# Performance work log

Measured on AMD Instinct MI355X. Metric: run time of the kernel, lower is better.

Reference implementation:

```python
import jax, jax.numpy as jnp
import numpy as np

B, S, D, H, HD = 2, 2048, 2048, 16, 128
MAX_TIMESCALE = 10000.0


def _fixed_pos_embedding(features, length, max_timescale):
    # flaxformer embedding.generate_fixed_pos_embedding
    fraction = jnp.arange(0, features, 2, dtype=jnp.float32) / features
    timescale = max_timescale ** fraction  # min_timescale = 1.0
    sinusoid = jnp.einsum('i,j->ij', jnp.arange(length, dtype=jnp.float32), 1.0 / timescale)
    sinusoid = jnp.concatenate([sinusoid, sinusoid], axis=-1)  # [length, features]
    return jnp.sin(sinusoid), jnp.cos(sinusoid)


def _rotate_half(x):
    x1, x2 = jnp.split(x, 2, axis=-1)
    return jnp.concatenate([-x2, x1], axis=-1)


def _apply_rope(x, sin, cos):
    # x: [B, S, H, HD]; sin/cos: [S, HD]
    sin = sin[None, :, None, :].astype(x.dtype)
    cos = cos[None, :, None, :].astype(x.dtype)
    return x * cos + _rotate_half(x) * sin


def setup_inputs() -> dict:
    key = jax.random.key(0)
    ks = jax.random.split(key, 6)
    inputs_q = jax.random.normal(ks[0], (B, S, D), dtype=jnp.float32)
    inputs_kv = jax.random.normal(ks[1], (B, S, D), dtype=jnp.float32)
    scale = D ** -0.5
    wq = jax.random.normal(ks[2], (D, H, HD), dtype=jnp.float32) * scale
    wk = jax.random.normal(ks[3], (D, H, HD), dtype=jnp.float32) * scale
    wv = jax.random.normal(ks[4], (D, H, HD), dtype=jnp.float32) * scale
    wo = jax.random.normal(ks[5], (H, HD, D), dtype=jnp.float32) * ((H * HD) ** -0.5)
    mask = jnp.tril(jnp.ones((S, S), dtype=bool))[None, None]  # causal [1,1,S,S]
    return {"inputs_q": inputs_q, "inputs_kv": inputs_kv, "wq": wq, "wk": wk,
            "wv": wv, "wo": wo, "mask": mask}


def reference(inputs_q, inputs_kv, wq, wk, wv, wo, mask):
    # QKV projections (split-head kernels) -> [B, S, H, HD]
    q = jnp.einsum('bqd,dhf->bqhf', inputs_q, wq)
    k = jnp.einsum('bkd,dhf->bkhf', inputs_kv, wk)
    v = jnp.einsum('bkd,dhf->bkhf', inputs_kv, wv)

    # Rotary embeddings applied to full head dim (fraction_to_rotate = 1.0)
    sin, cos = _fixed_pos_embedding(HD, S, MAX_TIMESCALE)
    q = _apply_rope(q, sin, cos)
    k = _apply_rope(k, sin, cos)

    # Logit rescaling by 1/sqrt(head_dim) (rescale_logits=False default path)
    q = q * (HD ** -0.5)

    logits = jnp.einsum('bqhf,bkhf->bhqk', q, k)  # [B, H, S, S]
    logits = jnp.where(mask, logits, jnp.asarray(-1e10, logits.dtype))
    probs = jax.nn.softmax(logits, axis=-1)

    ctx = jnp.einsum('bhqk,bkhf->bqhf', probs, v)
    out = jnp.einsum('bqhf,hfd->bqd', ctx, wo)  # output projection
    return out
```

## Files before the change

### kernel.cpp

```cpp
#include <hip/hip_runtime.h>

#define S_LEN 2048
#define NH 16
#define HDIM 128
#define DMODEL 2048

typedef __attribute__((ext_vector_type(8))) short bf16x8;
typedef __attribute__((ext_vector_type(4))) float f32x4;

using gas_cvp = const __attribute__((address_space(1))) void*;
using las_vp  = __attribute__((address_space(3))) void*;

__device__ __forceinline__ unsigned short f2bf(float x) {
  unsigned int u = __builtin_bit_cast(unsigned int, x);
  u += 0x7FFFu + ((u >> 16) & 1u);
  return (unsigned short)(u >> 16);
}
__device__ __forceinline__ float bf2f(unsigned short u) {
  unsigned int x = ((unsigned int)u) << 16;
  return __builtin_bit_cast(float, x);
}
__device__ __forceinline__ unsigned int cvt_pk_bf16(float lo, float hi) {
  unsigned int r;
  asm("v_cvt_pk_bf16_f32 %0, %1, %2" : "=v"(r) : "v"(lo), "v"(hi));
  return r;
}

__global__ __launch_bounds__(256) void cvt2_kernel(const float4* __restrict__ inq,
                                                   const float4* __restrict__ inkv,
                                                   ushort4* __restrict__ outq,
                                                   ushort4* __restrict__ outkv, int n4) {
  const float4* in = blockIdx.z ? inkv : inq;
  ushort4* out = blockIdx.z ? outkv : outq;
  int i = blockIdx.x * 256 + threadIdx.x;
  if (i < n4) {
    float4 v = in[i];
    ushort4 r;
    r.x = f2bf(v.x); r.y = f2bf(v.y); r.z = f2bf(v.z); r.w = f2bf(v.w);
    out[i] = r;
  }
}

__global__ __launch_bounds__(256) void sincos_kernel(float2* __restrict__ sc) {
  int i = blockIdx.x * 256 + threadIdx.x;
  int s = i >> 6, j = i & 63;
  float inv_ts = 1.0f / powf(10000.0f, (float)j * (1.0f / 64.0f));
  float ang = (float)s * inv_ts;
  sc[i] = make_float2(sinf(ang), cosf(ang));
}

__global__ __launch_bounds__(256) void rope8_kernel(const unsigned short* __restrict__ XQ,
                                                    const unsigned short* __restrict__ XK,
                                                    const float2* __restrict__ sc,
                                                    unsigned short* __restrict__ outQ,
                                                    unsigned short* __restrict__ outK,
                                                    float qscale) {
  const unsigned short* X = blockIdx.z ? XK : XQ;
  unsigned short* out = blockIdx.z ? outK : outQ;
  float scale = blockIdx.z ? 1.0f : qscale;
  int i = blockIdx.x * 256 + threadIdx.x;
  int m = i >> 7;
  int r = i & 127;
  int h = r >> 3, jb = (r & 7) * 8;
  int s = m & (S_LEN - 1);
  size_t base = (size_t)m * DMODEL + h * HDIM + jb;
  int4 x1 = *(const int4*)(X + base);
  int4 x2 = *(const int4*)(X + base + 64);
  const float2* pp = sc + s * 64 + jb;
  int4 o1, o2;
  int* x1w = (int*)&x1; int* x2w = (int*)&x2;
  int* o1w = (int*)&o1; int* o2w = (int*)&o2;
#pragma unroll
  for (int w = 0; w < 4; w++) {
    float a_lo = bf2f((unsigned short)(x1w[w] & 0xffff));
    float a_hi = bf2f((unsigned short)((unsigned int)x1w[w] >> 16));
    float b_lo = bf2f((unsigned short)(x2w[w] & 0xffff));
    float b_hi = bf2f((unsigned short)((unsigned int)x2w[w] >> 16));
    float2 c0 = pp[w * 2], c1 = pp[w * 2 + 1];
    float r1l = (a_lo * c0.y - b_lo * c0.x) * scale;
    float r1h = (a_hi * c1.y - b_hi * c1.x) * scale;
    float r2l = (b_lo * c0.y + a_lo * c0.x) * scale;
    float r2h = (b_hi * c1.y + a_hi * c1.x) * scale;
    o1w[w] = (int)(cvt_pk_bf16(r1l, r1h));
    o2w[w] = (int)(cvt_pk_bf16(r2l, r2h));
  }
  *(int4*)(out + base) = o1;
  *(int4*)(out + base + 64) = o2;
}

__global__ __launch_bounds__(256) void wtrans4_kernel(const float* __restrict__ w0,
                                                      const float* __restrict__ w1,
                                                      const float* __restrict__ w2,
                                                      const float* __restrict__ w3,
                                                      unsigned short* __restrict__ outb) {
  __shared__ float tile[64][65];
  int z = blockIdx.z;
  const float* in = (z == 0) ? w0 : (z == 1) ? w1 : (z == 2) ? w2 : w3;
  unsigned short* out = outb + (size_t)z * DMODEL * DMODEL;
  int c0 = blockIdx.x * 64, r0 = blockIdx.y * 64;
  int tx = threadIdx.x & 63, ty = threadIdx.x >> 6;
#pragma unroll
  for (int i = 0; i < 16; i++) {
    int r = ty + i * 4;
    tile[r][tx] = in[(size_t)(r0 + r) * DMODEL + c0 + tx];
  }
  __syncthreads();
#pragma unroll
  for (int i = 0; i < 16; i++) {
    int c = ty + i * 4;
    out[(size_t)(c0 + c) * DMODEL + r0 + tx] = f2bf(tile[tx][c]);
  }
}

__global__ __launch_bounds__(256) void vtrans_kernel(const unsigned short* __restrict__ vf,
                                                     unsigned short* __restrict__ Vt) {
  __shared__ unsigned short tile[64][65];
  int z = blockIdx.z; int b = z >> 4, h = z & 15;
  const unsigned short* I = vf + (size_t)b * S_LEN * DMODEL + h * HDIM;
  unsigned short* O = Vt + (size_t)z * HDIM * S_LEN;
  int s0 = blockIdx.y * 64, f0 = blockIdx.x * 64;
  int tx = threadIdx.x & 63, ty = threadIdx.x >> 6;
#pragma unroll
  for (int i = 0; i < 16; i++) {
    int r = ty + i * 4;
    tile[r][tx] = I[(size_t)(s0 + r) * DMODEL + f0 + tx];
  }
  __syncthreads();
#pragma unroll
  for (int i = 0; i < 16; i++) {
    int c = ty + i * 4;
    O[(size_t)(f0 + c) * S_LEN + s0 + tx] = tile[tx][c];
  }
}

__global__ __launch_bounds__(512, 1) void gemm256o_kernel(
    const unsigned short* __restrict__ Aq,
    const unsigned short* __restrict__ Akv,
    const unsigned short* __restrict__ W,
    unsigned short* __restrict__ Cb) {
  constexpr int M = 4096, N = 2048, K = 2048, NT = K / 64;
  __shared__ char lds[131072];
  int wid = blockIdx.z * 128 + blockIdx.y * 8 + blockIdx.x;
  int nid = (wid & 7) * 32 + (wid >> 3);
  int z = nid >> 7;
  int rem = nid & 127;
  int bm = (rem >> 3) * 256, bn = (rem & 7) * 256;
  const unsigned short* A = (z == 0) ? Aq : Akv;
  const unsigned short* Bt = W + (size_t)z * N * K;

  int tid = threadIdx.x, wave = tid >> 6, lane = tid & 63;
  int lr = lane & 15, lq = lane >> 4;
  int wr = wave >> 2, wc = wave & 3;

  auto STAGE_P = [&](int t, int buf, int isB) {
    int k0 = t * 64;
    const unsigned short* src = isB ? Bt : A;
    int rbase = isB ? bn : bm;
    char* dst0 = lds + buf * 65536 + isB * 32768;
#pragma unroll
    for (int i = 0; i < 4; i++) {
      int o = i * 8192 + tid * 16;
      int row = o >> 7, colb = o & 127;
      int sc = colb ^ ((row & 7) << 4);
      __builtin_amdgcn_global_load_lds(
          (gas_cvp)(src + (size_t)(rbase + row) * K + k0 + (sc >> 1)),
          (las_vp)(dst0 + i * 8192 + wave * 1024), 16, 0, 0);
    }
  };
  auto LDA1 = [&](int buf, int m, int kk) -> bf16x8 {
    int row = wr * 128 + m * 16 + lr;
    return *(const bf16x8*)(lds + buf * 65536 + row * 128 +
                            (((kk * 4 + lq) ^ (row & 7)) << 4));
  };
  auto LDB1 = [&](int buf, int n, int kk) -> bf16x8 {
    int row = wc * 64 + n * 16 + lr;
    return *(const bf16x8*)(lds + buf * 65536 + 32768 + row * 128 +
                            (((kk * 4 + lq) ^ (row & 7)) << 4));
  };

  f32x4 acc[8][4] = {};
  bf16x8 aA[4][2], bB[4][2];

  auto OCT = [&](int P, int Q, int sb) {
#pragma unroll
    for (int kk = 0; kk < 2; kk++)
#pragma unroll
      for (int s = 0; s < 2; s++)
#pragma unroll
        for (int nn = 0; nn < 2; nn++)
          acc[2 * P + s][2 * Q + nn] = __builtin_amdgcn_mfma_f32_16x16x32_bf16(
              aA[sb + s][kk], bB[2 * Q + nn][kk], acc[2 * P + s][2 * Q + nn], 0, 0, 0);
  };
  auto RD_A2 = [&](int buf, int m0, int sb) {
#pragma unroll
    for (int kk = 0; kk < 2; kk++)
#pragma unroll
      for (int s = 0; s < 2; s++) aA[sb + s][kk] = LDA1(buf, m0 + s, kk);
  };
  auto RD_B2 = [&](int buf, int n0) {
#pragma unroll
    for (int kk = 0; kk < 2; kk++)
#pragma unroll
      for (int s = 0; s < 2; s++) bB[n0 + s][kk] = LDB1(buf, n0 + s, kk);
  };

  STAGE_P(0, 0, 0); STAGE_P(0, 0, 1);
  asm volatile("s_waitcnt vmcnt(0)" ::: "memory");
  __builtin_amdgcn_sched_barrier(0);

  for (int T = 0; T < NT; T++) {
    int c = T & 1, nc = c ^ 1;
    __builtin_amdgcn_s_barrier();
    if (T + 1 < NT) { STAGE_P(T + 1, nc, 0); STAGE_P(T + 1, nc, 1); }
    __builtin_amdgcn_sched_barrier(0);
    RD_A2(c, 0, 0);
    __builtin_amdgcn_sched_barrier(0);
    RD_B2(c, 0);
    __builtin_amdgcn_sched_barrier(0);
    RD_B2(c, 2);
    __builtin_amdgcn_sched_barrier(0);
    RD_A2(c, 2, 2);
    __builtin_amdgcn_sched_barrier(0);

    asm volatile("s_waitcnt lgkmcnt(8)" ::: "memory");
    __builtin_amdgcn_sched_barrier(0);
    __builtin_amdgcn_s_setprio(1);
    OCT(0, 0, 0);
    __builtin_amdgcn_s_setprio(0);
    asm volatile("s_waitcnt lgkmcnt(4)" ::: "memory");
    __builtin_amdgcn_sched_barrier(0);
    __builtin_amdgcn_s_setprio(1);
    OCT(0, 1, 0);
    __builtin_amdgcn_s_setprio(0);
    RD_A2(c, 4, 0);
    __builtin_amdgcn_sched_barrier(0);
    asm volatile("s_waitcnt lgkmcnt(4)" ::: "memory");
    __builtin_amdgcn_sched_barrier(0);
    __builtin_amdgcn_s_setprio(1);
    OCT(1, 0, 2); OCT(1, 1, 2);
    __builtin_amdgcn_s_setprio(0);
    RD_A2(c, 6, 2);
    __builtin_amdgcn_sched_barrier(0);
    asm volatile("s_waitcnt lgkmcnt(4)" ::: "memory");
    __builtin_amdgcn_sched_barrier(0);
    __builtin_amdgcn_s_setprio(1);
    OCT(2, 0, 0); OCT(2, 1, 0);
    __builtin_amdgcn_s_setprio(0);
    asm volatile("s_waitcnt lgkmcnt(0)" ::: "memory");
    __builtin_amdgcn_sched_barrier(0);
    __builtin_amdgcn_s_setprio(1);
    OCT(3, 0, 2); OCT(3, 1, 2);
    __builtin_amdgcn_s_setprio(0);
    if (T + 1 < NT) {
      asm volatile("s_waitcnt vmcnt(0)" ::: "memory");
      __builtin_amdgcn_sched_barrier(0);
    }
  }
  asm volatile("s_waitcnt vmcnt(0) lgkmcnt(0)" ::: "memory");

  unsigned short* C = Cb + (size_t)z * M * N;
#pragma unroll
  for (int m = 0; m < 8; m++)
#pragma unroll
    for (int n = 0; n < 4; n++) {
      int row0 = bm + wr * 128 + m * 16 + lq * 4;
      int col = bn + wc * 64 + n * 16 + lr;
#pragma unroll
      for (int r = 0; r < 4; r++)
        C[(size_t)(row0 + r) * N + col] = f2bf(acc[m][n][r]);
    }
}

template <bool BF16OUT>
__global__ __launch_bounds__(512, 1) void gemmk_kernel(
    const unsigned short* __restrict__ Aq,
    const unsigned short* __restrict__ Akv,
    const unsigned short* __restrict__ W,
    void* __restrict__ Cb) {
  constexpr int M = 4096, N = 2048, K = 2048, NT = K / 64;
  __shared__ char lds[147456];
  int z = blockIdx.z;
  const unsigned short* A = (z == 0) ? Aq : Akv;
  const unsigned short* Bt = W + (size_t)z * N * K;

  int wid = blockIdx.y * 16 + blockIdx.x;
  int nid = (wid & 7) * 32 + (wid >> 3);
  int bn = (nid & 15) * 128, bm = (nid >> 4) * 256;

  int tid = threadIdx.x, wave = tid >> 6, lane = tid & 63;
  int lr = lane & 15, lq = lane >> 4;
  int wr = wave >> 1, wc = wave & 1;

  auto STAGE_U = [&](int t, int buf, int which) {
    int k0 = t * 64;
    const unsigned short* src = (which < 2) ? A : Bt;
    int rbase = (which < 2) ? (bm + which * 128) : bn;
    char* dst0 = lds + buf * 49152 + which * 16384;
#pragma unroll
    for (int i = 0; i < 2; i++) {
      int o = i * 8192 + wave * 1024 + lane * 16;
      int row = o >> 7, colb = o & 127;
      int sc = colb ^ ((row & 7) << 4);
      __builtin_amdgcn_global_load_lds(
          (gas_cvp)(src + (size_t)(rbase + row) * K + k0 + (sc >> 1)),
          (las_vp)(dst0 + i * 8192 + wave * 1024), 16, 0, 0);
    }
  };
  auto LDA = [&](int buf, int m, int kk) -> bf16x8 {
    int row = wr * 64 + m * 16 + lr;
    int half = row >> 7, r = row & 127;
    int byt = r * 128 + (((kk * 4 + lq) ^ (r & 7)) << 4);
    return *(const bf16x8*)(lds + buf * 49152 + half * 16384 + byt);
  };
  auto LDB = [&](int buf, int n, int kk) -> bf16x8 {
    int row = wc * 64 + n * 16 + lr;
    int byt = row * 128 + (((kk * 4 + lq) ^ (row & 7)) << 4);
    return *(const bf16x8*)(lds + buf * 49152 + 32768 + byt);
  };

  f32x4 acc[4][4] = {};
  bf16x8 aA[4][2], bB[4][2];

  auto QUAD = [&](int mg, int ng) {
#pragma unroll
    for (int kk = 0; kk < 2; kk++)
#pragma unroll
      for (int mm = 0; mm < 2; mm++)
#pragma unroll
        for (int nn = 0; nn < 2; nn++)
          acc[mg * 2 + mm][ng * 2 + nn] = __builtin_amdgcn_mfma_f32_16x16x32_bf16(
              aA[mg * 2 + mm][kk], bB[ng * 2 + nn][kk], acc[mg * 2 + mm][ng * 2 + nn], 0, 0, 0);
  };

  auto BODY = [&](int T, int cur, int dst, int mode) {
    __builtin_amdgcn_s_barrier();
    if (mode == 0) {
      STAGE_U(T + 2, dst, 0); STAGE_U(T + 2, dst, 1); STAGE_U(T + 2, dst, 2);
    }
    __builtin_amdgcn_sched_barrier(0);
#pragma unroll
    for (int kk = 0; kk < 2; kk++)
#pragma unroll
      for (int mm = 0; mm < 2; mm++) aA[mm][kk] = LDA(cur, mm, kk);
#pragma unroll
    for (int kk = 0; kk < 2; kk++)
#pragma unroll
      for (int nn = 0; nn < 2; nn++) bB[nn][kk] = LDB(cur, nn, kk);
    __builtin_amdgcn_sched_barrier(0);
#pragma unroll
    for (int kk = 0; kk < 2; kk++)
#pragma unroll
      for (int nn = 0; nn < 2; nn++) bB[2 + nn][kk] = LDB(cur, 2 + nn, kk);
    __builtin_amdgcn_sched_barrier(0);
#pragma unroll
    for (int kk = 0; kk < 2; kk++)
#pragma unroll
      for (int mm = 0; mm < 2; mm++) aA[2 + mm][kk] = LDA(cur, 2 + mm, kk);
    __builtin_amdgcn_sched_barrier(0);

    asm volatile("s_waitcnt lgkmcnt(8)" ::: "memory");
    __builtin_amdgcn_sched_barrier(0);
    __builtin_amdgcn_s_setprio(1);
    QUAD(0, 0);
    __builtin_amdgcn_s_setprio(0);
    asm volatile("s_waitcnt lgkmcnt(4)" ::: "memory");
    __builtin_amdgcn_sched_barrier(0);
    __builtin_amdgcn_s_setprio(1);
    QUAD(0, 1);
    __builtin_amdgcn_s_setprio(0);
    asm volatile("s_waitcnt lgkmcnt(0)" ::: "memory");
    __builtin_amdgcn_sched_barrier(0);
    __builtin_amdgcn_s_setprio(1);
    QUAD(1, 0); QUAD(1, 1);
    __builtin_amdgcn_s_setprio(0);
    if (mode == 0)      asm volatile("s_waitcnt vmcnt(6)" ::: "memory");
    else if (mode == 1) asm volatile("s_waitcnt vmcnt(0)" ::: "memory");
    __builtin_amdgcn_sched_barrier(0);
  };

  STAGE_U(0, 0, 0); STAGE_U(0, 0, 1); STAGE_U(0, 0, 2);
  STAGE_U(1, 1, 0); STAGE_U(1, 1, 1); STAGE_U(1, 1, 2);
  asm volatile("s_waitcnt vmcnt(6)" ::: "memory");
  __builtin_amdgcn_sched_barrier(0);

  int cur = 0;
  for (int T = 0; T < NT - 2; T++) {
    int dst = (cur == 0) ? 2 : cur - 1;
    BODY(T, cur, dst, 0);
    cur = (cur == 2) ? 0 : cur + 1;
  }
  BODY(NT - 2, cur, 0, 1);
  cur = (cur == 2) ? 0 : cur + 1;
  BODY(NT - 1, cur, 0, 2);
  asm volatile("s_waitcnt vmcnt(0) lgkmcnt(0)" ::: "memory");

#pragma unroll
  for (int m = 0; m < 4; m++)
#pragma unroll
    for (int n = 0; n < 4; n++) {
      int row0 = bm + wr * 64 + m * 16 + lq * 4;
      int col = bn + wc * 64 + n * 16 + lr;
      if (BF16OUT) {
        unsigned short* C = (unsigned short*)Cb;
#pragma unroll
        for (int r = 0; r < 4; r++)
          C[(size_t)(row0 + r) * N + col] = f2bf(acc[m][n][r]);
      } else {
        float* C = (float*)Cb;
#pragma unroll
        for (int r = 0; r < 4; r++)
          C[(size_t)(row0 + r) * N + col] = acc[m][n][r];
      }
    }
}

__global__ __launch_bounds__(512, 4) void attn_kernel(const unsigned short* __restrict__ Qb,
                                                      const unsigned short* __restrict__ Kb,
                                                      const unsigned short* __restrict__ Vt,
                                                      unsigned short* __restrict__ ctx) {
  __shared__ char lds[65536];
  int d = blockIdx.x;
  int hb = d & 31;
  int rank = d >> 5;
  int qtile = (rank < 8) ? (15 - rank) : (rank - 8);
  int h = hb & 15, b = hb >> 4;

  int tid = threadIdx.x, wave = tid >> 6, lane = tid & 63;
  int lr = lane & 15, lq = lane >> 4;
  int qw = qtile * 128 + wave * 16;
  int nt = 2 * qtile + 2;

  const unsigned short* Qp = Qb + (size_t)b * S_LEN * DMODEL + (size_t)h * HDIM;
  const unsigned short* Kp = Kb + (size_t)b * S_LEN * DMODEL + (size_t)h * HDIM;
  const unsigned short* Vp = Vt + (size_t)(b * NH + h) * HDIM * S_LEN;

  bf16x8 qa[4];
#pragma unroll
  for (int kf = 0; kf < 4; kf++)
    qa[kf] = *(const bf16x8*)(Qp + (size_t)(qw + lr) * DMODEL + kf * 32 + lq * 8);

  f32x4 o[8] = {};
  float mrow = -1e30f;
  float lsum = 0.f;
  bool hi = (lane >= 32);
  bool odd = (lq & 1);

  auto STAGE = [&](int tt, int bsel) {
    int kk0 = tt * 64;
#pragma unroll
    for (int i = 0; i < 2; i++) {
      int o_ = wave * 2048 + i * 1024 + lane * 16;
      int row = o_ >> 8, colb = o_ & 255;
      int sc_ = colb ^ ((row & 7) << 4);
      __builtin_amdgcn_global_load_lds(
          (gas_cvp)(Kp + (size_t)(kk0 + row) * DMODEL + (sc_ >> 1)),
          (las_vp)(lds + bsel * 32768 + wave * 2048 + i * 1024), 16, 0, 0);
    }
#pragma unroll
    for (int i = 0; i < 2; i++) {
      int o_ = wave * 2048 + i * 1024 + lane * 16;
      int row = o_ >> 7, colb = o_ & 127;
      int sc_ = colb ^ ((row & 7) << 4);
      __builtin_amdgcn_global_load_lds(
          (gas_cvp)(Vp + (size_t)row * S_LEN + kk0 + (sc_ >> 1)),
          (las_vp)(lds + bsel * 32768 + 16384 + wave * 2048 + i * 1024), 16, 0, 0);
    }
  };

  STAGE(0, 0);
  __syncthreads();

  for (int t = 0; t < nt; t++) {
    int cur = t & 1;
    int k0 = t * 64;
    if (t + 1 < nt) STAGE(t + 1, cur ^ 1);

    bool active = (k0 <= qw + 15);
    if (active) {
      const char* kbb = lds + cur * 32768;
      f32x4 sf[4] = {};
#pragma unroll
      for (int kf = 0; kf < 4; kf++) {
        bf16x8 kbf[4];
#pragma unroll
        for (int nf = 0; nf < 4; nf++) {
          int row = nf * 16 + lr;
          int colb = kf * 64 + lq * 16;
          kbf[nf] = *(const bf16x8*)(kbb + row * 256 + (colb ^ ((row & 7) << 4)));
        }
#pragma unroll
        for (int nf = 0; nf < 4; nf++)
          sf[nf] = __builtin_amdgcn_mfma_f32_16x16x32_bf16(kbf[nf], qa[kf], sf[nf], 0, 0, 0);
      }

      if (k0 + 63 > qw) {
        int q = qw + lr;
#pragma unroll
        for (int nf = 0; nf < 4; nf++)
#pragma unroll
          for (int r = 0; r < 4; r++)
            if (k0 + nf * 16 + lq * 4 + r > q) sf[nf][r] = -1e30f;
      }

      float v = sf[0][0];
#pragma unroll
      for (int nf = 0; nf < 4; nf++)
#pragma unroll
        for (int r = 0; r < 4; r++) v = fmaxf(v, sf[nf][r]);
      v = fmaxf(v, __shfl_xor(v, 16));
      v = fmaxf(v, __shfl_xor(v, 32));
      bool need = (v > mrow + 8.f);
      if (__any(need)) {
        float mn = fmaxf(mrow, v);
        float al = exp2f(mrow - mn);
        mrow = mn;
        lsum *= al;
#pragma unroll
        for (int ff = 0; ff < 8; ff++) o[ff] *= al;
      }
      float rs = 0.f;
#pragma unroll
      for (int nf = 0; nf < 4; nf++)
#pragma unroll
        for (int r = 0; r < 4; r++) {
          float p = exp2f(sf[nf][r] - mrow);
          sf[nf][r] = p;
          rs += p;
        }
      rs += __shfl_xor(rs, 16);
      rs += __shfl_xor(rs, 32);
      lsum += rs;

      const char* vbb = lds + cur * 32768 + 16384;
#pragma unroll
      for (int c = 0; c < 2; c++) {
        unsigned int A0 = cvt_pk_bf16(sf[2 * c][0], sf[2 * c][1]);
        unsigned int A1 = cvt_pk_bf16(sf[2 * c][2], sf[2 * c][3]);
        unsigned int B0 = cvt_pk_bf16(sf[2 * c + 1][0], sf[2 * c + 1][1]);
        unsigned int B1 = cvt_pk_bf16(sf[2 * c + 1][2], sf[2 * c + 1][3]);
        unsigned int sA0 = (unsigned int)__shfl_xor((int)A0, 32);
        unsigned int sA1 = (unsigned int)__shfl_xor((int)A1, 32);
        unsigned int sB0 = (unsigned int)__shfl_xor((int)B0, 32);
        unsigned int sB1 = (unsigned int)__shfl_xor((int)B1, 32);
        unsigned int Y0f = hi ? sB0 : A0, Y0s = hi ? B0 : sA0;
        unsigned int Y1f = hi ? sB1 : A1, Y1s = hi ? B1 : sA1;
        unsigned int z0 = odd ? Y0f : Y0s, z1 = odd ? Y1f : Y1s;
        unsigned int w0 = (unsigned int)__shfl_xor((int)z0, 16);
        unsigned int w1 = (unsigned int)__shfl_xor((int)z1, 16);
        int4 fr;
        fr.x = (int)(odd ? w0 : Y0f);
        fr.y = (int)(odd ? w1 : Y1f);
        fr.z = (int)(odd ? Y0s : w0);
        fr.w = (int)(odd ? Y1s : w1);
        bf16x8 pfrag = __builtin_bit_cast(bf16x8, fr);
#pragma unroll
        for (int ff = 0; ff < 8; ff++) {
          int row = ff * 16 + lr;
          int colb = c * 64 + lq * 16;
          bf16x8 vb = *(const bf16x8*)(vbb + row * 128 + (colb ^ ((row & 7) << 4)));
          o[ff] = __builtin_amdgcn_mfma_f32_16x16x32_bf16(vb, pfrag, o[ff], 0, 0, 0);
        }
      }
    }

    __syncthreads();
  }

  float inv = 1.0f / lsum;
  size_t rb = ((size_t)b * S_LEN + qw + lr) * DMODEL + h * HDIM;
#pragma unroll
  for (int ff = 0; ff < 8; ff++) {
    unsigned int u0 = cvt_pk_bf16(o[ff][0] * inv, o[ff][1] * inv);
    unsigned int u1 = cvt_pk_bf16(o[ff][2] * inv, o[ff][3] * inv);
    *(uint2*)(ctx + rb + ff * 16 + lq * 4) = make_uint2(u0, u1);
  }
}

extern "C" void kernel_launch(void* const* d_in, const int* in_sizes, int n_in,
                              void* d_out, int out_size, void* d_ws, size_t ws_size,
                              hipStream_t stream) {
  const float* inq  = (const float*)d_in[0];
  const float* inkv = (const float*)d_in[1];
  const float* wq   = (const float*)d_in[2];
  const float* wk   = (const float*)d_in[3];
  const float* wv   = (const float*)d_in[4];
  const float* wo   = (const float*)d_in[5];
  float* out = (float*)d_out;

  char* ws = (char*)d_ws;
  const size_t MB = 1ull << 20;
  unsigned short* xq  = (unsigned short*)(ws);
  unsigned short* xkv = (unsigned short*)(ws + 16 * MB);
  unsigned short* wqt = (unsigned short*)(ws + 32 * MB);
  unsigned short* wvt = (unsigned short*)(ws + 48 * MB);
  unsigned short* wot = (unsigned short*)(ws + 56 * MB);
  float2* sc          = (float2*)(ws + 64 * MB);
  unsigned short* projb = (unsigned short*)(ws + 66 * MB);
  unsigned short* Vt   = (unsigned short*)(ws + 114 * MB);
  unsigned short* ctxb = (unsigned short*)(ws + 130 * MB);
  unsigned short* Qb = xq;
  unsigned short* Kb = xkv;

  const int n4 = (2 * S_LEN * DMODEL) / 4;
  cvt2_kernel<<<dim3(n4 / 256, 1, 2), 256, 0, stream>>>(
      (const float4*)inq, (const float4*)inkv, (ushort4*)xq, (ushort4*)xkv, n4);

  wtrans4_kernel<<<dim3(32, 32, 4), 256, 0, stream>>>(wq, wk, wv, wo, wqt);

  sincos_kernel<<<(S_LEN * 64) / 256, 256, 0, stream>>>(sc);

  const float qscale = 0.12751743249052045f;
  unsigned short* projQ = projb;
  unsigned short* projK = projb + (size_t)4096 * 2048;
  unsigned short* projV = projb + (size_t)2 * 4096 * 2048;

  gemm256o_kernel<<<dim3(8, 16, 2), 512, 0, stream>>>(xq, xkv, wqt, projb);
  gemmk_kernel<true><<<dim3(16, 16, 1), 512, 0, stream>>>(xkv, xkv, wvt, (void*)projV);

  rope8_kernel<<<dim3(2048, 1, 2), 256, 0, stream>>>(projQ, projK, sc, Qb, Kb, qscale);
  vtrans_kernel<<<dim3(2, 32, 32), 256, 0, stream>>>(projV, Vt);

  attn_kernel<<<512, 512, 0, stream>>>(Qb, Kb, Vt, ctxb);

  gemmk_kernel<false><<<dim3(16, 16, 1), 512, 0, stream>>>(ctxb, ctxb, wot, (void*)out);
}
```

Measured before the change: 259.5 us.

## Switch GEMMs to 32x32x16 MFMA tiles and compute softmax row sums via MFMA

Both projection GEMM kernels move from 16x16x32 to 32x32x16 bf16 MFMA fragments. Each K-step is restructured into alternating X/Y register fragment sets, and the LDS swizzle now also XORs in row bits 3-4, so the wider fragment reads do not hit bank conflicts. Larger MFMA tiles cut the number of LDS fragment loads per FLOP. In attention, the per-row softmax sum is computed with an extra MFMA against a ones vector instead of scalar adds and cross-lane shuffles. The epilogue store layouts change to the 32x32 accumulator layout, and the wider accumulators raise register pressure.

```diff
diff --git a/kernel.cpp b/kernel.cpp
--- a/kernel.cpp
+++ b/kernel.cpp
@@ -7,6 +7,7 @@
 
 typedef __attribute__((ext_vector_type(8))) short bf16x8;
 typedef __attribute__((ext_vector_type(4))) float f32x4;
+typedef __attribute__((ext_vector_type(16))) float f32x16;
 
 using gas_cvp = const __attribute__((address_space(1))) void*;
 using las_vp  = __attribute__((address_space(3))) void*;
@@ -24,6 +25,9 @@
   unsigned int r;
   asm("v_cvt_pk_bf16_f32 %0, %1, %2" : "=v"(r) : "v"(lo), "v"(hi));
   return r;
+}
+__device__ __forceinline__ int gswz(int row) {
+  return (((row & 7) ^ ((row >> 3) & 3)) << 4);
 }
 
 __global__ __launch_bounds__(256) void cvt2_kernel(const float4* __restrict__ inq,
@@ -149,7 +153,7 @@
   const unsigned short* Bt = W + (size_t)z * N * K;
 
   int tid = threadIdx.x, wave = tid >> 6, lane = tid & 63;
-  int lr = lane & 15, lq = lane >> 4;
+  int l31 = lane & 31, l5 = lane >> 5;
   int wr = wave >> 2, wc = wave & 3;
 
   auto STAGE_P = [&](int t, int buf, int isB) {
@@ -161,47 +165,51 @@
     for (int i = 0; i < 4; i++) {
       int o = i * 8192 + tid * 16;
       int row = o >> 7, colb = o & 127;
-      int sc = colb ^ ((row & 7) << 4);
+      int sc = colb ^ gswz(row);
       __builtin_amdgcn_global_load_lds(
           (gas_cvp)(src + (size_t)(rbase + row) * K + k0 + (sc >> 1)),
           (las_vp)(dst0 + i * 8192 + wave * 1024), 16, 0, 0);
     }
   };
-  auto LDA1 = [&](int buf, int m, int kk) -> bf16x8 {
-    int row = wr * 128 + m * 16 + lr;
-    return *(const bf16x8*)(lds + buf * 65536 + row * 128 +
-                            (((kk * 4 + lq) ^ (row & 7)) << 4));
-  };
-  auto LDB1 = [&](int buf, int n, int kk) -> bf16x8 {
-    int row = wc * 64 + n * 16 + lr;
-    return *(const bf16x8*)(lds + buf * 65536 + 32768 + row * 128 +
-                            (((kk * 4 + lq) ^ (row & 7)) << 4));
-  };
-
-  f32x4 acc[8][4] = {};
-  bf16x8 aA[4][2], bB[4][2];
-
-  auto OCT = [&](int P, int Q, int sb) {
-#pragma unroll
-    for (int kk = 0; kk < 2; kk++)
-#pragma unroll
-      for (int s = 0; s < 2; s++)
-#pragma unroll
-        for (int nn = 0; nn < 2; nn++)
-          acc[2 * P + s][2 * Q + nn] = __builtin_amdgcn_mfma_f32_16x16x32_bf16(
-              aA[sb + s][kk], bB[2 * Q + nn][kk], acc[2 * P + s][2 * Q + nn], 0, 0, 0);
-  };
-  auto RD_A2 = [&](int buf, int m0, int sb) {
-#pragma unroll
-    for (int kk = 0; kk < 2; kk++)
-#pragma unroll
-      for (int s = 0; s < 2; s++) aA[sb + s][kk] = LDA1(buf, m0 + s, kk);
-  };
-  auto RD_B2 = [&](int buf, int n0) {
-#pragma unroll
-    for (int kk = 0; kk < 2; kk++)
-#pragma unroll
-      for (int s = 0; s < 2; s++) bB[n0 + s][kk] = LDB1(buf, n0 + s, kk);
+  auto LDA1 = [&](int buf, int fm, int kf) -> bf16x8 {
+    int row = wr * 128 + fm * 32 + l31;
+    int kb = kf * 32 + l5 * 16;
+    return *(const bf16x8*)(lds + buf * 65536 + row * 128 + (kb ^ gswz(row)));
+  };
+  auto LDB1 = [&](int buf, int fn, int kf) -> bf16x8 {
+    int row = wc * 64 + fn * 32 + l31;
+    int kb = kf * 32 + l5 * 16;
+    return *(const bf16x8*)(lds + buf * 65536 + 32768 + row * 128 + (kb ^ gswz(row)));
+  };
+
+  f32x16 acc[4][2] = {};
+  bf16x8 aX[4], bX[2], aY[4], bY[2];
+
+  auto RDX = [&](int buf, int kf) {
+#pragma unroll
+    for (int fm = 0; fm < 4; fm++) aX[fm] = LDA1(buf, fm, kf);
+#pragma unroll
+    for (int fn = 0; fn < 2; fn++) bX[fn] = LDB1(buf, fn, kf);
+  };
+  auto RDY = [&](int buf, int kf) {
+#pragma unroll
+    for (int fm = 0; fm < 4; fm++) aY[fm] = LDA1(buf, fm, kf);
+#pragma unroll
+    for (int fn = 0; fn < 2; fn++) bY[fn] = LDB1(buf, fn, kf);
+  };
+  auto MFX = [&]() {
+#pragma unroll
+    for (int fm = 0; fm < 4; fm++)
+#pragma unroll
+      for (int fn = 0; fn < 2; fn++)
+        acc[fm][fn] = __builtin_amdgcn_mfma_f32_32x32x16_bf16(aX[fm], bX[fn], acc[fm][fn], 0, 0, 0);
+  };
+  auto MFY = [&]() {
+#pragma unroll
+    for (int fm = 0; fm < 4; fm++)
+#pragma unroll
+      for (int fn = 0; fn < 2; fn++)
+        acc[fm][fn] = __builtin_amdgcn_mfma_f32_32x32x16_bf16(aY[fm], bY[fn], acc[fm][fn], 0, 0, 0);
   };
 
   STAGE_P(0, 0, 0); STAGE_P(0, 0, 1);
@@ -213,44 +221,27 @@
     __builtin_amdgcn_s_barrier();
     if (T + 1 < NT) { STAGE_P(T + 1, nc, 0); STAGE_P(T + 1, nc, 1); }
     __builtin_amdgcn_sched_barrier(0);
-    RD_A2(c, 0, 0);
-    __builtin_amdgcn_sched_barrier(0);
-    RD_B2(c, 0);
-    __builtin_amdgcn_sched_barrier(0);
-    RD_B2(c, 2);
-    __builtin_amdgcn_sched_barrier(0);
-    RD_A2(c, 2, 2);
-    __builtin_amdgcn_sched_barrier(0);
-
-    asm volatile("s_waitcnt lgkmcnt(8)" ::: "memory");
-    __builtin_amdgcn_sched_barrier(0);
-    __builtin_amdgcn_s_setprio(1);
-    OCT(0, 0, 0);
-    __builtin_amdgcn_s_setprio(0);
-    asm volatile("s_waitcnt lgkmcnt(4)" ::: "memory");
-    __builtin_amdgcn_sched_barrier(0);
-    __builtin_amdgcn_s_setprio(1);
-    OCT(0, 1, 0);
-    __builtin_amdgcn_s_setprio(0);
-    RD_A2(c, 4, 0);
-    __builtin_amdgcn_sched_barrier(0);
-    asm volatile("s_waitcnt lgkmcnt(4)" ::: "memory");
-    __builtin_amdgcn_sched_barrier(0);
-    __builtin_amdgcn_s_setprio(1);
-    OCT(1, 0, 2); OCT(1, 1, 2);
-    __builtin_amdgcn_s_setprio(0);
-    RD_A2(c, 6, 2);
-    __builtin_amdgcn_sched_barrier(0);
-    asm volatile("s_waitcnt lgkmcnt(4)" ::: "memory");
-    __builtin_amdgcn_sched_barrier(0);
-    __builtin_amdgcn_s_setprio(1);
-    OCT(2, 0, 0); OCT(2, 1, 0);
-    __builtin_amdgcn_s_setprio(0);
+    RDX(c, 0);
+    __builtin_amdgcn_sched_barrier(0);
+    RDY(c, 1);
+    __builtin_amdgcn_sched_barrier(0);
+
+    asm volatile("s_waitcnt lgkmcnt(6)" ::: "memory");
+    __builtin_amdgcn_sched_barrier(0);
+    __builtin_amdgcn_s_setprio(1); MFX(); __builtin_amdgcn_s_setprio(0);
+    RDX(c, 2);
+    __builtin_amdgcn_sched_barrier(0);
+    asm volatile("s_waitcnt lgkmcnt(6)" ::: "memory");
+    __builtin_amdgcn_sched_barrier(0);
+    __builtin_amdgcn_s_setprio(1); MFY(); __builtin_amdgcn_s_setprio(0);
+    RDY(c, 3);
+    __builtin_amdgcn_sched_barrier(0);
+    asm volatile("s_waitcnt lgkmcnt(6)" ::: "memory");
+    __builtin_amdgcn_sched_barrier(0);
+    __builtin_amdgcn_s_setprio(1); MFX(); __builtin_amdgcn_s_setprio(0);
     asm volatile("s_waitcnt lgkmcnt(0)" ::: "memory");
     __builtin_amdgcn_sched_barrier(0);
-    __builtin_amdgcn_s_setprio(1);
-    OCT(3, 0, 2); OCT(3, 1, 2);
-    __builtin_amdgcn_s_setprio(0);
+    __builtin_amdgcn_s_setprio(1); MFY(); __builtin_amdgcn_s_setprio(0);
     if (T + 1 < NT) {
       asm volatile("s_waitcnt vmcnt(0)" ::: "memory");
       __builtin_amdgcn_sched_barrier(0);
@@ -260,15 +251,15 @@
 
   unsigned short* C = Cb + (size_t)z * M * N;
 #pragma unroll
-  for (int m = 0; m < 8; m++)
-#pragma unroll
-    for (int n = 0; n < 4; n++) {
-      int row0 = bm + wr * 128 + m * 16 + lq * 4;
-      int col = bn + wc * 64 + n * 16 + lr;
-#pragma unroll
-      for (int r = 0; r < 4; r++)
-        C[(size_t)(row0 + r) * N + col] = f2bf(acc[m][n][r]);
-    }
+  for (int fm = 0; fm < 4; fm++)
+#pragma unroll
+    for (int fn = 0; fn < 2; fn++)
+#pragma unroll
+      for (int reg = 0; reg < 16; reg++) {
+        int row = bm + wr * 128 + fm * 32 + (reg & 3) + 8 * (reg >> 2) + 4 * l5;
+        int col = bn + wc * 64 + fn * 32 + l31;
+        C[(size_t)row * N + col] = f2bf(acc[fm][fn][reg]);
+      }
 }
 
 template <bool BF16OUT>
@@ -288,7 +279,7 @@
   int bn = (nid & 15) * 128, bm = (nid >> 4) * 256;
 
   int tid = threadIdx.x, wave = tid >> 6, lane = tid & 63;
-  int lr = lane & 15, lq = lane >> 4;
+  int l31 = lane & 31, l5 = lane >> 5;
   int wr = wave >> 1, wc = wave & 1;
 
   auto STAGE_U = [&](int t, int buf, int which) {
@@ -300,36 +291,52 @@
     for (int i = 0; i < 2; i++) {
       int o = i * 8192 + wave * 1024 + lane * 16;
       int row = o >> 7, colb = o & 127;
-      int sc = colb ^ ((row & 7) << 4);
+      int sc = colb ^ gswz(row);
       __builtin_amdgcn_global_load_lds(
           (gas_cvp)(src + (size_t)(rbase + row) * K + k0 + (sc >> 1)),
           (las_vp)(dst0 + i * 8192 + wave * 1024), 16, 0, 0);
     }
   };
-  auto LDA = [&](int buf, int m, int kk) -> bf16x8 {
-    int row = wr * 64 + m * 16 + lr;
+  auto LDA = [&](int buf, int fm, int kf) -> bf16x8 {
+    int row = wr * 64 + fm * 32 + l31;
     int half = row >> 7, r = row & 127;
-    int byt = r * 128 + (((kk * 4 + lq) ^ (r & 7)) << 4);
-    return *(const bf16x8*)(lds + buf * 49152 + half * 16384 + byt);
-  };
-  auto LDB = [&](int buf, int n, int kk) -> bf16x8 {
-    int row = wc * 64 + n * 16 + lr;
-    int byt = row * 128 + (((kk * 4 + lq) ^ (row & 7)) << 4);
-    return *(const bf16x8*)(lds + buf * 49152 + 32768 + byt);
-  };
-
-  f32x4 acc[4][4] = {};
-  bf16x8 aA[4][2], bB[4][2];
-
-  auto QUAD = [&](int mg, int ng) {
-#pragma unroll
-    for (int kk = 0; kk < 2; kk++)
-#pragma unroll
-      for (int mm = 0; mm < 2; mm++)
-#pragma unroll
-        for (int nn = 0; nn < 2; nn++)
-          acc[mg * 2 + mm][ng * 2 + nn] = __builtin_amdgcn_mfma_f32_16x16x32_bf16(
-              aA[mg * 2 + mm][kk], bB[ng * 2 + nn][kk], acc[mg * 2 + mm][ng * 2 + nn], 0, 0, 0);
+    int kb = kf * 32 + l5 * 16;
+    return *(const bf16x8*)(lds + buf * 49152 + half * 16384 + r * 128 + (kb ^ gswz(r)));
+  };
+  auto LDB = [&](int buf, int fn, int kf) -> bf16x8 {
+    int row = wc * 64 + fn * 32 + l31;
+    int kb = kf * 32 + l5 * 16;
+    return *(const bf16x8*)(lds + buf * 49152 + 32768 + row * 128 + (kb ^ gswz(row)));
+  };
+
+  f32x16 acc[2][2] = {};
+  bf16x8 aX[2], bX[2], aY[2], bY[2];
+
+  auto RDX = [&](int buf, int kf) {
+#pragma unroll
+    for (int fm = 0; fm < 2; fm++) aX[fm] = LDA(buf, fm, kf);
+#pragma unroll
+    for (int fn = 0; fn < 2; fn++) bX[fn] = LDB(buf, fn, kf);
+  };
+  auto RDY = [&](int buf, int kf) {
+#pragma unroll
+    for (int fm = 0; fm < 2; fm++) aY[fm] = LDA(buf, fm, kf);
+#pragma unroll
+    for (int fn = 0; fn < 2; fn++) bY[fn] = LDB(buf, fn, kf);
+  };
+  auto MFX = [&]() {
+#pragma unroll
+    for (int fm = 0; fm < 2; fm++)
+#pragma unroll
+      for (int fn = 0; fn < 2; fn++)
+        acc[fm][fn] = __builtin_amdgcn_mfma_f32_32x32x16_bf16(aX[fm], bX[fn], acc[fm][fn], 0, 0, 0);
+  };
+  auto MFY = [&]() {
+#pragma unroll
+    for (int fm = 0; fm < 2; fm++)
+#pragma unroll
+      for (int fn = 0; fn < 2; fn++)
+        acc[fm][fn] = __builtin_amdgcn_mfma_f32_32x32x16_bf16(aY[fm], bY[fn], acc[fm][fn], 0, 0, 0);
   };
 
   auto BODY = [&](int T, int cur, int dst, int mode) {
@@ -338,41 +345,27 @@
       STAGE_U(T + 2, dst, 0); STAGE_U(T + 2, dst, 1); STAGE_U(T + 2, dst, 2);
     }
     __builtin_amdgcn_sched_barrier(0);
-#pragma unroll
-    for (int kk = 0; kk < 2; kk++)
-#pragma unroll
-      for (int mm = 0; mm < 2; mm++) aA[mm][kk] = LDA(cur, mm, kk);
-#pragma unroll
-    for (int kk = 0; kk < 2; kk++)
-#pragma unroll
-      for (int nn = 0; nn < 2; nn++) bB[nn][kk] = LDB(cur, nn, kk);
-    __builtin_amdgcn_sched_barrier(0);
-#pragma unroll
-    for (int kk = 0; kk < 2; kk++)
-#pragma unroll
-      for (int nn = 0; nn < 2; nn++) bB[2 + nn][kk] = LDB(cur, 2 + nn, kk);
-    __builtin_amdgcn_sched_barrier(0);
-#pragma unroll
-    for (int kk = 0; kk < 2; kk++)
-#pragma unroll
-      for (int mm = 0; mm < 2; mm++) aA[2 + mm][kk] = LDA(cur, 2 + mm, kk);
-    __builtin_amdgcn_sched_barrier(0);
-
-    asm volatile("s_waitcnt lgkmcnt(8)" ::: "memory");
-    __builtin_amdgcn_sched_barrier(0);
-    __builtin_amdgcn_s_setprio(1);
-    QUAD(0, 0);
-    __builtin_amdgcn_s_setprio(0);
+    RDX(cur, 0);
+    __builtin_amdgcn_sched_barrier(0);
+    RDY(cur, 1);
+    __builtin_amdgcn_sched_barrier(0);
+
     asm volatile("s_waitcnt lgkmcnt(4)" ::: "memory");
     __builtin_amdgcn_sched_barrier(0);
-    __builtin_amdgcn_s_setprio(1);
-    QUAD(0, 1);
-    __builtin_amdgcn_s_setprio(0);
+    __builtin_amdgcn_s_setprio(1); MFX(); __builtin_amdgcn_s_setprio(0);
+    RDX(cur, 2);
+    __builtin_amdgcn_sched_barrier(0);
+    asm volatile("s_waitcnt lgkmcnt(4)" ::: "memory");
+    __builtin_amdgcn_sched_barrier(0);
+    __builtin_amdgcn_s_setprio(1); MFY(); __builtin_amdgcn_s_setprio(0);
+    RDY(cur, 3);
+    __builtin_amdgcn_sched_barrier(0);
+    asm volatile("s_waitcnt lgkmcnt(4)" ::: "memory");
+    __builtin_amdgcn_sched_barrier(0);
+    __builtin_amdgcn_s_setprio(1); MFX(); __builtin_amdgcn_s_setprio(0);
     asm volatile("s_waitcnt lgkmcnt(0)" ::: "memory");
     __builtin_amdgcn_sched_barrier(0);
-    __builtin_amdgcn_s_setprio(1);
-    QUAD(1, 0); QUAD(1, 1);
-    __builtin_amdgcn_s_setprio(0);
+    __builtin_amdgcn_s_setprio(1); MFY(); __builtin_amdgcn_s_setprio(0);
     if (mode == 0)      asm volatile("s_waitcnt vmcnt(6)" ::: "memory");
     else if (mode == 1) asm volatile("s_waitcnt vmcnt(0)" ::: "memory");
     __builtin_amdgcn_sched_barrier(0);
@@ -395,23 +388,18 @@
   asm volatile("s_waitcnt vmcnt(0) lgkmcnt(0)" ::: "memory");
 
 #pragma unroll
-  for (int m = 0; m < 4; m++)
-#pragma unroll
-    for (int n = 0; n < 4; n++) {
-      int row0 = bm + wr * 64 + m * 16 + lq * 4;
-      int col = bn + wc * 64 + n * 16 + lr;
-      if (BF16OUT) {
-        unsigned short* C = (unsigned short*)Cb;
-#pragma unroll
-        for (int r = 0; r < 4; r++)
-          C[(size_t)(row0 + r) * N + col] = f2bf(acc[m][n][r]);
-      } else {
-        float* C = (float*)Cb;
-#pragma unroll
-        for (int r = 0; r < 4; r++)
-          C[(size_t)(row0 + r) * N + col] = acc[m][n][r];
+  for (int fm = 0; fm < 2; fm++)
+#pragma unroll
+    for (int fn = 0; fn < 2; fn++)
+#pragma unroll
+      for (int reg = 0; reg < 16; reg++) {
+        int row = bm + wr * 64 + fm * 32 + (reg & 3) + 8 * (reg >> 2) + 4 * l5;
+        int col = bn + wc * 64 + fn * 32 + l31;
+        if (BF16OUT)
+          ((unsigned short*)Cb)[(size_t)row * N + col] = f2bf(acc[fm][fn][reg]);
+        else
+          ((float*)Cb)[(size_t)row * N + col] = acc[fm][fn][reg];
       }
-    }
 }
 
 __global__ __launch_bounds__(512, 4) void attn_kernel(const unsigned short* __restrict__ Qb,
@@ -439,9 +427,12 @@
   for (int kf = 0; kf < 4; kf++)
     qa[kf] = *(const bf16x8*)(Qp + (size_t)(qw + lr) * DMODEL + kf * 32 + lq * 8);
 
+  int4 onesi = make_int4(0x3F803F80, 0x3F803F80, 0x3F803F80, 0x3F803F80);
+  bf16x8 ones8 = __builtin_bit_cast(bf16x8, onesi);
+
   f32x4 o[8] = {};
+  f32x4 osum = {};
   float mrow = -1e30f;
-  float lsum = 0.f;
   bool hi = (lane >= 32);
   bool odd = (lq & 1);
 
@@ -514,22 +505,15 @@
         float mn = fmaxf(mrow, v);
         float al = exp2f(mrow - mn);
         mrow = mn;
-        lsum *= al;
+        osum *= al;
 #pragma unroll
         for (int ff = 0; ff < 8; ff++) o[ff] *= al;
       }
-      float rs = 0.f;
 #pragma unroll
       for (int nf = 0; nf < 4; nf++)
 #pragma unroll
-        for (int r = 0; r < 4; r++) {
-          float p = exp2f(sf[nf][r] - mrow);
-          sf[nf][r] = p;
-          rs += p;
-        }
-      rs += __shfl_xor(rs, 16);
-      rs += __shfl_xor(rs, 32);
-      lsum += rs;
+        for (int r = 0; r < 4; r++)
+          sf[nf][r] = exp2f(sf[nf][r] - mrow);
 
       const char* vbb = lds + cur * 32768 + 16384;
 #pragma unroll
@@ -553,6 +537,7 @@
         fr.z = (int)(odd ? Y0s : w0);
         fr.w = (int)(odd ? Y1s : w1);
         bf16x8 pfrag = __builtin_bit_cast(bf16x8, fr);
+        osum = __builtin_amdgcn_mfma_f32_16x16x32_bf16(ones8, pfrag, osum, 0, 0, 0);
 #pragma unroll
         for (int ff = 0; ff < 8; ff++) {
           int row = ff * 16 + lr;
@@ -566,7 +551,7 @@
     __syncthreads();
   }
 
-  float inv = 1.0f / lsum;
+  float inv = 1.0f / osum[0];
   size_t rb = ((size_t)b * S_LEN + qw + lr) * DMODEL + h * HDIM;
 #pragma unroll
   for (int ff = 0; ff < 8; ff++) {
```

Result: slower. 272.0 us (+4.8%).

## Shrink attention q-tiles to 64 rows, read V from global, sum rows via MFMA

Applied to the files above, without the earlier changes.

The attention kernel moves from 128-query tiles with 8 waves to 64-query tiles with 4 waves, doubling the grid and halving LDS use. Only K is staged in LDS; V fragments are loaded straight from global memory into registers. The per-row softmax denominator is now accumulated by an extra MFMA against a ones vector instead of shuffle reductions. This targets idle waves on causal tiles and LDS pressure, and may allow more blocks per CU. The cost is uncoalesced-ish global V reads repeated per wave and bf16 rounding in the row-sum.

```diff
diff --git a/kernel.cpp b/kernel.cpp
--- a/kernel.cpp
+++ b/kernel.cpp
@@ -414,21 +414,21 @@
     }
 }
 
-__global__ __launch_bounds__(512, 4) void attn_kernel(const unsigned short* __restrict__ Qb,
+__global__ __launch_bounds__(256, 4) void attn_kernel(const unsigned short* __restrict__ Qb,
                                                       const unsigned short* __restrict__ Kb,
                                                       const unsigned short* __restrict__ Vt,
                                                       unsigned short* __restrict__ ctx) {
-  __shared__ char lds[65536];
+  __shared__ char lds[32768];
   int d = blockIdx.x;
   int hb = d & 31;
   int rank = d >> 5;
-  int qtile = (rank < 8) ? (15 - rank) : (rank - 8);
+  int qtile = 31 - rank;
   int h = hb & 15, b = hb >> 4;
 
   int tid = threadIdx.x, wave = tid >> 6, lane = tid & 63;
   int lr = lane & 15, lq = lane >> 4;
-  int qw = qtile * 128 + wave * 16;
-  int nt = 2 * qtile + 2;
+  int qw = qtile * 64 + wave * 16;
+  int nt = qtile + 1;
 
   const unsigned short* Qp = Qb + (size_t)b * S_LEN * DMODEL + (size_t)h * HDIM;
   const unsigned short* Kp = Kb + (size_t)b * S_LEN * DMODEL + (size_t)h * HDIM;
@@ -439,134 +439,119 @@
   for (int kf = 0; kf < 4; kf++)
     qa[kf] = *(const bf16x8*)(Qp + (size_t)(qw + lr) * DMODEL + kf * 32 + lq * 8);
 
+  int4 onesi = make_int4(0x3F803F80, 0x3F803F80, 0x3F803F80, 0x3F803F80);
+  bf16x8 ones8 = __builtin_bit_cast(bf16x8, onesi);
+
   f32x4 o[8] = {};
+  f32x4 osum = {};
   float mrow = -1e30f;
-  float lsum = 0.f;
   bool hi = (lane >= 32);
   bool odd = (lq & 1);
 
-  auto STAGE = [&](int tt, int bsel) {
+  auto STAGE_K = [&](int tt, int bsel) {
     int kk0 = tt * 64;
 #pragma unroll
-    for (int i = 0; i < 2; i++) {
-      int o_ = wave * 2048 + i * 1024 + lane * 16;
+    for (int i = 0; i < 4; i++) {
+      int o_ = i * 4096 + tid * 16;
       int row = o_ >> 8, colb = o_ & 255;
       int sc_ = colb ^ ((row & 7) << 4);
       __builtin_amdgcn_global_load_lds(
           (gas_cvp)(Kp + (size_t)(kk0 + row) * DMODEL + (sc_ >> 1)),
-          (las_vp)(lds + bsel * 32768 + wave * 2048 + i * 1024), 16, 0, 0);
-    }
-#pragma unroll
-    for (int i = 0; i < 2; i++) {
-      int o_ = wave * 2048 + i * 1024 + lane * 16;
-      int row = o_ >> 7, colb = o_ & 127;
-      int sc_ = colb ^ ((row & 7) << 4);
-      __builtin_amdgcn_global_load_lds(
-          (gas_cvp)(Vp + (size_t)row * S_LEN + kk0 + (sc_ >> 1)),
-          (las_vp)(lds + bsel * 32768 + 16384 + wave * 2048 + i * 1024), 16, 0, 0);
-    }
-  };
-
-  STAGE(0, 0);
+          (las_vp)(lds + bsel * 16384 + i * 4096 + wave * 1024), 16, 0, 0);
+    }
+  };
+
+  STAGE_K(0, 0);
   __syncthreads();
 
   for (int t = 0; t < nt; t++) {
     int cur = t & 1;
     int k0 = t * 64;
-    if (t + 1 < nt) STAGE(t + 1, cur ^ 1);
-
-    bool active = (k0 <= qw + 15);
-    if (active) {
-      const char* kbb = lds + cur * 32768;
-      f32x4 sf[4] = {};
-#pragma unroll
-      for (int kf = 0; kf < 4; kf++) {
-        bf16x8 kbf[4];
-#pragma unroll
-        for (int nf = 0; nf < 4; nf++) {
-          int row = nf * 16 + lr;
-          int colb = kf * 64 + lq * 16;
-          kbf[nf] = *(const bf16x8*)(kbb + row * 256 + (colb ^ ((row & 7) << 4)));
-        }
-#pragma unroll
-        for (int nf = 0; nf < 4; nf++)
-          sf[nf] = __builtin_amdgcn_mfma_f32_16x16x32_bf16(kbf[nf], qa[kf], sf[nf], 0, 0, 0);
+    if (t + 1 < nt) STAGE_K(t + 1, cur ^ 1);
+
+    const char* kbb = lds + cur * 16384;
+    f32x4 sf[4] = {};
+#pragma unroll
+    for (int kf = 0; kf < 4; kf++) {
+      bf16x8 kbf[4];
+#pragma unroll
+      for (int nf = 0; nf < 4; nf++) {
+        int row = nf * 16 + lr;
+        int colb = kf * 64 + lq * 16;
+        kbf[nf] = *(const bf16x8*)(kbb + row * 256 + (colb ^ ((row & 7) << 4)));
       }
-
-      if (k0 + 63 > qw) {
-        int q = qw + lr;
-#pragma unroll
-        for (int nf = 0; nf < 4; nf++)
-#pragma unroll
-          for (int r = 0; r < 4; r++)
-            if (k0 + nf * 16 + lq * 4 + r > q) sf[nf][r] = -1e30f;
-      }
-
-      float v = sf[0][0];
 #pragma unroll
       for (int nf = 0; nf < 4; nf++)
-#pragma unroll
-        for (int r = 0; r < 4; r++) v = fmaxf(v, sf[nf][r]);
-      v = fmaxf(v, __shfl_xor(v, 16));
-      v = fmaxf(v, __shfl_xor(v, 32));
-      bool need = (v > mrow + 8.f);
-      if (__any(need)) {
-        float mn = fmaxf(mrow, v);
-        float al = exp2f(mrow - mn);
-        mrow = mn;
-        lsum *= al;
-#pragma unroll
-        for (int ff = 0; ff < 8; ff++) o[ff] *= al;
-      }
-      float rs = 0.f;
+        sf[nf] = __builtin_amdgcn_mfma_f32_16x16x32_bf16(kbf[nf], qa[kf], sf[nf], 0, 0, 0);
+    }
+
+    if (k0 + 63 > qw) {
+      int q = qw + lr;
 #pragma unroll
       for (int nf = 0; nf < 4; nf++)
 #pragma unroll
-        for (int r = 0; r < 4; r++) {
-          float p = exp2f(sf[nf][r] - mrow);
-          sf[nf][r] = p;
-          rs += p;
-        }
-      rs += __shfl_xor(rs, 16);
-      rs += __shfl_xor(rs, 32);
-      lsum += rs;
-
-      const char* vbb = lds + cur * 32768 + 16384;
-#pragma unroll
-      for (int c = 0; c < 2; c++) {
-        unsigned int A0 = cvt_pk_bf16(sf[2 * c][0], sf[2 * c][1]);
-        unsigned int A1 = cvt_pk_bf16(sf[2 * c][2], sf[2 * c][3]);
-        unsigned int B0 = cvt_pk_bf16(sf[2 * c + 1][0], sf[2 * c + 1][1]);
-        unsigned int B1 = cvt_pk_bf16(sf[2 * c + 1][2], sf[2 * c + 1][3]);
-        unsigned int sA0 = (unsigned int)__shfl_xor((int)A0, 32);
-        unsigned int sA1 = (unsigned int)__shfl_xor((int)A1, 32);
-        unsigned int sB0 = (unsigned int)__shfl_xor((int)B0, 32);
-        unsigned int sB1 = (unsigned int)__shfl_xor((int)B1, 32);
-        unsigned int Y0f = hi ? sB0 : A0, Y0s = hi ? B0 : sA0;
-        unsigned int Y1f = hi ? sB1 : A1, Y1s = hi ? B1 : sA1;
-        unsigned int z0 = odd ? Y0f : Y0s, z1 = odd ? Y1f : Y1s;
-        unsigned int w0 = (unsigned int)__shfl_xor((int)z0, 16);
-        unsigned int w1 = (unsigned int)__shfl_xor((int)z1, 16);
-        int4 fr;
-        fr.x = (int)(odd ? w0 : Y0f);
-        fr.y = (int)(odd ? w1 : Y1f);
-        fr.z = (int)(odd ? Y0s : w0);
-        fr.w = (int)(odd ? Y1s : w1);
-        bf16x8 pfrag = __builtin_bit_cast(bf16x8, fr);
-#pragma unroll
-        for (int ff = 0; ff < 8; ff++) {
-          int row = ff * 16 + lr;
-          int colb = c * 64 + lq * 16;
-          bf16x8 vb = *(const bf16x8*)(vbb + row * 128 + (colb ^ ((row & 7) << 4)));
-          o[ff] = __builtin_amdgcn_mfma_f32_16x16x32_bf16(vb, pfrag, o[ff], 0, 0, 0);
-        }
-      }
+        for (int r = 0; r < 4; r++)
+          if (k0 + nf * 16 + lq * 4 + r > q) sf[nf][r] = -1e30f;
+    }
+
+    float v = sf[0][0];
+#pragma unroll
+    for (int nf = 0; nf < 4; nf++)
+#pragma unroll
+      for (int r = 0; r < 4; r++) v = fmaxf(v, sf[nf][r]);
+    v = fmaxf(v, __shfl_xor(v, 16));
+    v = fmaxf(v, __shfl_xor(v, 32));
+    bool need = (v > mrow + 8.f);
+    if (__any(need)) {
+      float mn = fmaxf(mrow, v);
+      float al = exp2f(mrow - mn);
+      mrow = mn;
+      osum *= al;
+#pragma unroll
+      for (int ff = 0; ff < 8; ff++) o[ff] *= al;
+    }
+#pragma unroll
+    for (int nf = 0; nf < 4; nf++)
+#pragma unroll
+      for (int r = 0; r < 4; r++)
+        sf[nf][r] = exp2f(sf[nf][r] - mrow);
+
+#pragma unroll
+    for (int c = 0; c < 2; c++) {
+      bf16x8 vbank[8];
+#pragma unroll
+      for (int ff = 0; ff < 8; ff++)
+        vbank[ff] = *(const bf16x8*)(Vp + (size_t)(ff * 16 + lr) * S_LEN + k0 + c * 32 + lq * 8);
+
+      unsigned int A0 = cvt_pk_bf16(sf[2 * c][0], sf[2 * c][1]);
+      unsigned int A1 = cvt_pk_bf16(sf[2 * c][2], sf[2 * c][3]);
+      unsigned int B0 = cvt_pk_bf16(sf[2 * c + 1][0], sf[2 * c + 1][1]);
+      unsigned int B1 = cvt_pk_bf16(sf[2 * c + 1][2], sf[2 * c + 1][3]);
+      unsigned int sA0 = (unsigned int)__shfl_xor((int)A0, 32);
+      unsigned int sA1 = (unsigned int)__shfl_xor((int)A1, 32);
+      unsigned int sB0 = (unsigned int)__shfl_xor((int)B0, 32);
+      unsigned int sB1 = (unsigned int)__shfl_xor((int)B1, 32);
+      unsigned int Y0f = hi ? sB0 : A0, Y0s = hi ? B0 : sA0;
+      unsigned int Y1f = hi ? sB1 : A1, Y1s = hi ? B1 : sA1;
+      unsigned int z0 = odd ? Y0f : Y0s, z1 = odd ? Y1f : Y1s;
+      unsigned int w0 = (unsigned int)__shfl_xor((int)z0, 16);
+      unsigned int w1 = (unsigned int)__shfl_xor((int)z1, 16);
+      int4 fr;
+      fr.x = (int)(odd ? w0 : Y0f);
+      fr.y = (int)(odd ? w1 : Y1f);
+      fr.z = (int)(odd ? Y0s : w0);
+      fr.w = (int)(odd ? Y1s : w1);
+      bf16x8 pfrag = __builtin_bit_cast(bf16x8, fr);
+      osum = __builtin_amdgcn_mfma_f32_16x16x32_bf16(ones8, pfrag, osum, 0, 0, 0);
+#pragma unroll
+      for (int ff = 0; ff < 8; ff++)
+        o[ff] = __builtin_amdgcn_mfma_f32_16x16x32_bf16(vbank[ff], pfrag, o[ff], 0, 0, 0);
     }
 
     __syncthreads();
   }
 
-  float inv = 1.0f / lsum;
+  float inv = 1.0f / osum[0];
   size_t rb = ((size_t)b * S_LEN + qw + lr) * DMODEL + h * HDIM;
 #pragma unroll
   for (int ff = 0; ff < 8; ff++) {
@@ -620,7 +605,7 @@
   rope8_kernel<<<dim3(2048, 1, 2), 256, 0, stream>>>(projQ, projK, sc, Qb, Kb, qscale);
   vtrans_kernel<<<dim3(2, 32, 32), 256, 0, stream>>>(projV, Vt);
 
-  attn_kernel<<<512, 512, 0, stream>>>(Qb, Kb, Vt, ctxb);
+  attn_kernel<<<1024, 256, 0, stream>>>(Qb, Kb, Vt, ctxb);
 
   gemmk_kernel<false><<<dim3(16, 16, 1), 512, 0, stream>>>(ctxb, ctxb, wot, (void*)out);
 }
```

After: 399.6 us. 54.0% more time.
